# Performance work log

Hardware: AMD Instinct MI355X
Metric: run time of the kernel (lower is better)

Reference implementation:

```python
import jax, jax.numpy as jnp
import numpy as np

B, C, L, O = 32, 256, 336, 96
K, NLAYERS, DFF = 4, 2, 1024
EPS = 1e-5


def setup_inputs() -> dict:
    key = jax.random.key(0)
    ks = jax.random.split(key, 10)
    s1 = 1.0 / np.sqrt(L)
    s2 = 1.0 / np.sqrt(DFF)
    return {
        "x": jax.random.normal(ks[0], (B, C, L), dtype=jnp.float32),
        "rev_w": jnp.ones((C,), dtype=jnp.float32),
        "rev_b": jnp.zeros((C,), dtype=jnp.float32),
        "W1": jax.random.normal(ks[1], (K, NLAYERS, L, DFF), dtype=jnp.float32) * s1,
        "b1": jnp.zeros((K, NLAYERS, DFF), dtype=jnp.float32),
        "W2": jax.random.normal(ks[2], (K, NLAYERS, DFF, L), dtype=jnp.float32) * s2,
        "b2": jnp.zeros((K, NLAYERS, L), dtype=jnp.float32),
        "Wh": jax.random.normal(ks[3], (K, L, O), dtype=jnp.float32) * s1,
        "bh": jnp.zeros((K, O), dtype=jnp.float32),
        "assign": jax.random.randint(ks[4], (C,), 0, K, dtype=jnp.int32),
    }


def reference(x, rev_w, rev_b, W1, b1, W2, b2, Wh, bh, assign):
    # RevIN norm over the time axis, per instance and per channel. x: [B,C,L]
    mean = jnp.mean(x, axis=-1, keepdims=True)
    std = jnp.sqrt(jnp.var(x, axis=-1, keepdims=True) + EPS)
    xn = (x - mean) / std * rev_w[None, :, None] + rev_b[None, :, None]

    n_clusters = Wh.shape[0]
    n_layers = W1.shape[1]
    out = jnp.zeros(x.shape[:2] + (Wh.shape[-1],), dtype=x.dtype)  # [B,C,O]
    for k in range(n_clusters):
        z = xn  # [B,C,L] time-mixing MLP stack shared across channels
        for l in range(n_layers):
            h = jax.nn.relu(jnp.einsum('bcl,ld->bcd', z, W1[k, l]) + b1[k, l])
            z = z + jnp.einsum('bcd,dl->bcl', h, W2[k, l]) + b2[k, l]
        y = jnp.einsum('bcl,lo->bco', z, Wh[k]) + bh[k]  # [B,C,O]
        out = jnp.where((assign == k)[None, :, None], y, out)

    # RevIN denorm, then transpose to [B, out_len, C]
    out = (out - rev_b[None, :, None]) / rev_w[None, :, None] * std + mean
    return jnp.transpose(out, (0, 2, 1))
```

## Files before the change

kernel.cpp:

```cpp
#include <hip/hip_runtime.h>
#include <math.h>


typedef unsigned short u16;
typedef unsigned int u32;
typedef unsigned long long u64;

constexpr int B = 32, C = 256, L = 336, O = 96, K = 4, NL = 2, DFF = 1024;
constexpr int TM = 32;
constexpr int NTILES = (B * C) / TM;
constexpr int LP = 352;
constexpr int ZBS = 360;
constexpr int HS = 1032;

constexpr int DT1 = 32;
constexpr int KT1 = 22;
constexpr int LT2 = 11;
constexpr int KT2 = 64;
constexpr int NTH = 6;
constexpr int KSH = 11;

constexpr int TS1 = KT1 * 512;
constexpr int TS2 = KT2 * 512;
constexpr int THS = KSH * 512;

constexpr int W1FRAGS = DT1 * KT1 * 64;
constexpr int W2FRAGS = LT2 * KT2 * 64;
constexpr int WHFRAGS = NTH * KSH * 64;
constexpr int NW1 = W1FRAGS * K * NL;
constexpr int NW2 = W2FRAGS * K * NL;
constexpr int NPREP = 176 + 256 + 44 + 1;

typedef __bf16 bf16x8 __attribute__((ext_vector_type(8)));
typedef float f32x4 __attribute__((ext_vector_type(4)));
typedef float f32x16 __attribute__((ext_vector_type(16)));

__device__ __forceinline__ u16 f2bf(float f) {
  union { float f; u32 u; } v;
  v.f = f;
  u32 r = v.u + 0x7fffu + ((v.u >> 16) & 1u);
  return (u16)(r >> 16);
}
__device__ __forceinline__ float bf2f(u16 h) {
  union { u32 u; float f; } v;
  v.u = ((u32)h) << 16;
  return v.f;
}
__device__ __forceinline__ u32 pack2(float a, float b) {
  return (u32)f2bf(a) | ((u32)f2bf(b) << 16);
}

__global__ __launch_bounds__(256) void prep(const int* __restrict__ assign,
                                            const float* __restrict__ W1,
                                            const float* __restrict__ W2,
                                            const float* __restrict__ Wh,
                                            int* __restrict__ meta,
                                            u16* __restrict__ wbuf) {
  __shared__ u16 sm[32][516];
  const int bid = blockIdx.x;
  const int tid = threadIdx.x;
  const int wid = tid >> 6, lane = tid & 63;
  const int q = lane >> 4, rm = lane & 15;
  const int q2 = lane >> 5, n32 = lane & 31;

  if (bid < 176) {
    const int dh = bid & 1;
    const int ks32 = (bid >> 1) % 11;
    const int kl = bid / 22;
    for (int rr = 0; rr < 8; ++rr) {
      const int r = wid * 8 + rr;
      const int l = ks32 * 32 + r;
#pragma unroll
      for (int h = 0; h < 2; ++h) {
        const int c = h * 256 + lane * 4;
        float4 v = make_float4(0.f, 0.f, 0.f, 0.f);
        if (l < L)
          v = *(const float4*)(W1 + ((size_t)kl * L + l) * DFF + dh * 512 + c);
        uint2 p;
        p.x = pack2(v.x, v.y);
        p.y = pack2(v.z, v.w);
        *(uint2*)&sm[r][c] = p;
      }
    }
    __syncthreads();
    for (int e = 0; e < 8; ++e) {
      const int item = wid * 8 + e;
      const int dtl = item >> 1, half = item & 1;
      const int rb = 16 * half + q2 * 8;
      const int col = dtl * 32 + n32;
      uint4 o;
      u32 w4[4];
#pragma unroll
      for (int jj = 0; jj < 4; ++jj)
        w4[jj] = (u32)sm[rb + 2 * jj][col] | ((u32)sm[rb + 2 * jj + 1][col] << 16);
      o.x = w4[0]; o.y = w4[1]; o.z = w4[2]; o.w = w4[3];
      const int dt = dh * 16 + dtl;
      const int ks = ks32 * 2 + half;
      *(uint4*)(wbuf + ((size_t)(kl * DT1 + dt) * KT1 + ks) * 512 + lane * 8) = o;
    }
  } else if (bid < 432) {
    const int b2i = bid - 176;
    const int ks32 = b2i & 31;
    const int kl = b2i >> 5;
    for (int rr = 0; rr < 8; ++rr) {
      const int r = wid * 8 + rr;
      const float* row = W2 + ((size_t)kl * DFF + ks32 * 32 + r) * L;
      {
        const int c = lane * 4;
        const float4 v = *(const float4*)(row + c);
        uint2 p;
        p.x = pack2(v.x, v.y);
        p.y = pack2(v.z, v.w);
        *(uint2*)&sm[r][c] = p;
      }
      {
        const int c = 256 + lane * 4;
        if (c < 352) {
          float4 v = make_float4(0.f, 0.f, 0.f, 0.f);
          if (c < L) v = *(const float4*)(row + c);
          uint2 p;
          p.x = pack2(v.x, v.y);
          p.y = pack2(v.z, v.w);
          *(uint2*)&sm[r][c] = p;
        }
      }
    }
    __syncthreads();
    for (int item = wid; item < 22; item += 4) {
      const int lt = item >> 1, half = item & 1;
      const int rb = 16 * half + q2 * 8;
      const int col = 32 * lt + n32;
      uint4 o;
      u32 w4[4];
#pragma unroll
      for (int jj = 0; jj < 4; ++jj)
        w4[jj] = (u32)sm[rb + 2 * jj][col] | ((u32)sm[rb + 2 * jj + 1][col] << 16);
      o.x = w4[0]; o.y = w4[1]; o.z = w4[2]; o.w = w4[3];
      const int ks = ks32 * 2 + half;
      *(uint4*)(wbuf + (size_t)NW1 * 8 +
                ((size_t)(kl * LT2 + lt) * KT2 + ks) * 512 + lane * 8) = o;
    }
  } else if (bid < 476) {
    const int b3i = bid - 432;
    const int ks = b3i % 11;
    const int kk = b3i / 11;
    for (int rr = 0; rr < 8; ++rr) {
      const int r = wid * 8 + rr;
      const int l = ks * 32 + r;
      if (lane < 24) {
        const int c = lane * 4;
        float4 v = make_float4(0.f, 0.f, 0.f, 0.f);
        if (l < L) v = *(const float4*)(Wh + ((size_t)kk * L + l) * O + c);
        uint2 p;
        p.x = pack2(v.x, v.y);
        p.y = pack2(v.z, v.w);
        *(uint2*)&sm[r][c] = p;
      }
    }
    __syncthreads();
    for (int nt = wid; nt < NTH; nt += 4) {
      uint4 o;
      u32 w4[4];
#pragma unroll
      for (int jj = 0; jj < 4; ++jj) {
        const u16 a = sm[q * 8 + 2 * jj][nt * 16 + rm];
        const u16 b = sm[q * 8 + 2 * jj + 1][nt * 16 + rm];
        w4[jj] = (u32)a | ((u32)b << 16);
      }
      o.x = w4[0]; o.y = w4[1]; o.z = w4[2]; o.w = w4[3];
      *(uint4*)(wbuf + (size_t)(NW1 + NW2) * 8 +
                ((size_t)(kk * NTH + nt) * KSH + ks) * 512 + lane * 8) = o;
    }
  } else {
    __shared__ int wcnt[4][K];
    __shared__ int pre[4][K];
    __shared__ int cofs[K + 1];
    const int a = assign[tid];
    const u64 below = (1ull << lane) - 1ull;
    int myrank = 0;
#pragma unroll
    for (int k = 0; k < K; ++k) {
      const u64 m = __ballot(a == k);
      if (a == k) myrank = (int)__popcll(m & below);
      if (lane == 0) wcnt[wid][k] = (int)__popcll(m);
    }
    __syncthreads();
    if (tid == 0) {
      int tot[K];
      for (int k = 0; k < K; ++k) {
        int s = 0;
        for (int ww = 0; ww < 4; ++ww) {
          pre[ww][k] = s;
          s += wcnt[ww][k];
        }
        tot[k] = s;
      }
      cofs[0] = 0;
      for (int k = 0; k < K; ++k) cofs[k + 1] = cofs[k] + tot[k];
      for (int k = 0; k <= K; ++k) meta[512 + k] = cofs[k];
    }
    __syncthreads();
    const int pos = cofs[a] + pre[wid][a] + myrank;
    meta[256 + pos] = tid;
    int k = 0;
    while (k < K - 1 && tid >= cofs[k + 1]) ++k;
    meta[tid] = (k << 16) | ((tid - cofs[k]) * TM);
  }
}

__global__ __launch_bounds__(1024, 4) void mlp_mfma(
    const float* __restrict__ x, const float* __restrict__ rev_w,
    const float* __restrict__ rev_b, const float* __restrict__ b1,
    const float* __restrict__ b2, const float* __restrict__ bh,
    const int* __restrict__ meta, const u16* __restrict__ wbuf,
    float* __restrict__ out) {
  __shared__ __align__(16) u16 zb[TM][ZBS];
  __shared__ __align__(16) u16 Hsh[TM][HS];
  __shared__ float s_mean[TM], s_std[TM], s_rw[TM], s_rb[TM];
  __shared__ int s_b[TM], s_c[TM];

  const int tid = threadIdx.x;
  const int wid = tid >> 6;
  const int lane = tid & 63;
  const int q = lane >> 4, rm = lane & 15;
  const int q2 = lane >> 5, n32 = lane & 31;

  const int swz = (blockIdx.x & 7) * 32 + (blockIdx.x >> 3);
  const int info = meta[swz];
  const int kcl = info >> 16;
  const int rstart = info & 0xffff;
  const int cofs = meta[512 + kcl];
  const int cnt = meta[512 + kcl + 1] - cofs;

  for (int i = 0; i < 2; ++i) {
    const int t = wid * 2 + i;
    const int ri = rstart + t;
    const int b = ri / cnt;
    const int c = meta[256 + cofs + (ri % cnt)];
    const float* xrow = x + (size_t)(b * C + c) * L;
    float v[6], s = 0.f, s2 = 0.f;
#pragma unroll
    for (int jj = 0; jj < 6; ++jj) {
      const int j = lane + jj * 64;
      v[jj] = (j < L) ? xrow[j] : 0.f;
      s += v[jj];
      s2 += v[jj] * v[jj];
    }
#pragma unroll
    for (int off = 32; off > 0; off >>= 1) {
      s += __shfl_down(s, off);
      s2 += __shfl_down(s2, off);
    }
    s = __shfl(s, 0);
    s2 = __shfl(s2, 0);
    const float mean = s * (1.f / L);
    const float var = s2 * (1.f / L) - mean * mean;
    const float stdv = sqrtf(var + 1e-5f);
    const float rstd = 1.f / stdv;
    const float rw = rev_w[c], rb_ = rev_b[c];
#pragma unroll
    for (int jj = 0; jj < 6; ++jj) {
      const int j = lane + jj * 64;
      if (j < L) zb[t][j] = f2bf((v[jj] - mean) * rstd * rw + rb_);
    }
    if (lane < LP - L) zb[t][L + lane] = 0;
    if (lane == 0) {
      s_mean[t] = mean;
      s_std[t] = stdv;
      s_rw[t] = rw;
      s_rb[t] = rb_;
      s_b[t] = b;
      s_c[t] = c;
    }
  }

  const u16* w1b = wbuf;
  const u16* w2b = wbuf + (size_t)NW1 * 8;
  const u16* whb = wbuf + (size_t)(NW1 + NW2) * 8;

  bf16x8 a1[2][4];
  {
    const u16* b0 = w1b + (size_t)(kcl * NL) * W1FRAGS * 8 +
                    (size_t)(wid * 2) * TS1 + lane * 8;
#pragma unroll
    for (int t = 0; t < 2; ++t)
#pragma unroll
      for (int s = 0; s < 4; ++s)
        a1[t][s] = *(const bf16x8*)(b0 + (size_t)t * TS1 + s * 512);
  }
  __syncthreads();

  f32x16 zm;
#pragma unroll
  for (int i = 0; i < 16; ++i) zm[i] = 0.f;
  if (wid < LT2) {
#pragma unroll
    for (int g = 0; g < 4; ++g) {
      const uint2 zw = *(const uint2*)&zb[n32][32 * wid + 8 * g + 4 * q2];
      zm[4 * g + 0] = bf2f((u16)zw.x);
      zm[4 * g + 1] = bf2f((u16)(zw.x >> 16));
      zm[4 * g + 2] = bf2f((u16)zw.y);
      zm[4 * g + 3] = bf2f((u16)(zw.y >> 16));
    }
  }

  for (int l = 0; l < NL; ++l) {
    const int kl = kcl * NL + l;
    const u16* W1f = w1b + (size_t)kl * W1FRAGS * 8;
    const u16* W2f = w2b + (size_t)kl * W2FRAGS * 8;
    const float* b1p = b1 + kl * DFF;
    const float* b2p = b2 + kl * L;
    const u16* base1 = W1f + (size_t)(wid * 2) * TS1 + lane * 8;

    f32x16 acc[2];
#pragma unroll
    for (int t = 0; t < 2; ++t)
#pragma unroll
      for (int i = 0; i < 16; ++i) acc[t][i] = 0.f;
#pragma unroll
    for (int ks = 0; ks < KT1; ++ks) {
      const bf16x8 zf = *(const bf16x8*)&zb[n32][ks * 16 + q2 * 8];
#pragma unroll
      for (int t = 0; t < 2; ++t)
        acc[t] = __builtin_amdgcn_mfma_f32_32x32x16_bf16(a1[t][ks & 3], zf,
                                                         acc[t], 0, 0, 0);
      if (ks + 4 < KT1) {
#pragma unroll
        for (int t = 0; t < 2; ++t)
          a1[t][ks & 3] =
              *(const bf16x8*)(base1 + (size_t)t * TS1 + (ks + 4) * 512);
      }
    }
#pragma unroll
    for (int t = 0; t < 2; ++t) {
      const int dt = wid * 2 + t;
#pragma unroll
      for (int g = 0; g < 4; ++g) {
        const int db = dt * 32 + 8 * g + 4 * q2;
        const float4 bq = *(const float4*)(b1p + db);
        uint2 hw;
        hw.x = pack2(fmaxf(acc[t][4 * g + 0] + bq.x, 0.f),
                     fmaxf(acc[t][4 * g + 1] + bq.y, 0.f));
        hw.y = pack2(fmaxf(acc[t][4 * g + 2] + bq.z, 0.f),
                     fmaxf(acc[t][4 * g + 3] + bq.w, 0.f));
        *(uint2*)&Hsh[n32][db] = hw;
      }
    }

    bf16x8 a2[8];
    const u16* base2 = W2f + (size_t)wid * TS2 + lane * 8;
    if (wid < LT2) {
#pragma unroll
      for (int s = 0; s < 8; ++s)
        a2[s] = *(const bf16x8*)(base2 + s * 512);
    }
    __syncthreads();

    if (wid < LT2) {
#pragma unroll
      for (int ks = 0; ks < KT2; ++ks) {
        const bf16x8 hf = *(const bf16x8*)&Hsh[n32][ks * 16 + q2 * 8];
        zm = __builtin_amdgcn_mfma_f32_32x32x16_bf16(a2[ks & 7], hf, zm, 0, 0, 0);
        if (ks + 8 < KT2)
          a2[ks & 7] = *(const bf16x8*)(base2 + (ks + 8) * 512);
      }
#pragma unroll
      for (int g = 0; g < 4; ++g) {
        const int lc = 32 * wid + 8 * g + 4 * q2;
        if (lc < L) {
          const float4 bq = *(const float4*)(b2p + lc);
          zm[4 * g + 0] += bq.x;
          zm[4 * g + 1] += bq.y;
          zm[4 * g + 2] += bq.z;
          zm[4 * g + 3] += bq.w;
        }
        uint2 zw;
        zw.x = pack2(zm[4 * g + 0], zm[4 * g + 1]);
        zw.y = pack2(zm[4 * g + 2], zm[4 * g + 3]);
        *(uint2*)&zb[n32][lc] = zw;
      }
    }

    if (l + 1 < NL) {
      const u16* nb = w1b + (size_t)(kl + 1) * W1FRAGS * 8 +
                      (size_t)(wid * 2) * TS1 + lane * 8;
#pragma unroll
      for (int t = 0; t < 2; ++t)
#pragma unroll
        for (int s = 0; s < 4; ++s)
          a1[t][s] = *(const bf16x8*)(nb + (size_t)t * TS1 + s * 512);
    }
    __syncthreads();
  }

  if (wid < NTH) {
    const u16* Whf =
        whb + (size_t)kcl * WHFRAGS * 8 + (size_t)wid * THS + lane * 8;
    f32x4 acc0 = {0.f, 0.f, 0.f, 0.f}, acc1 = {0.f, 0.f, 0.f, 0.f};
    for (int ks = 0; ks < KSH; ++ks) {
      const bf16x8 af = *(const bf16x8*)(Whf + ks * 512);
      const bf16x8 zf0 = *(const bf16x8*)&zb[rm][ks * 32 + q * 8];
      const bf16x8 zf1 = *(const bf16x8*)&zb[rm + 16][ks * 32 + q * 8];
      acc0 = __builtin_amdgcn_mfma_f32_16x16x32_bf16(af, zf0, acc0, 0, 0, 0);
      acc1 = __builtin_amdgcn_mfma_f32_16x16x32_bf16(af, zf1, acc1, 0, 0, 0);
    }
    const float4 bq = *(const float4*)(bh + kcl * O + wid * 16 + q * 4);
    const float bqa[4] = {bq.x, bq.y, bq.z, bq.w};
#pragma unroll
    for (int rg = 0; rg < 2; ++rg) {
      const int row = rm + 16 * rg;
      const float mean = s_mean[row], stdv = s_std[row];
      const float rw = s_rw[row], rb_ = s_rb[row];
      const int ob = s_b[row], oc = s_c[row];
      const f32x4 acc = rg ? acc1 : acc0;
#pragma unroll
      for (int gg = 0; gg < 4; ++gg) {
        const int o = wid * 16 + q * 4 + gg;
        const float y = acc[gg] + bqa[gg];
        out[((size_t)ob * O + o) * C + oc] = (y - rb_) / rw * stdv + mean;
      }
    }
  }
}

extern "C" void kernel_launch(void* const* d_in, const int* in_sizes, int n_in,
                              void* d_out, int out_size, void* d_ws,
                              size_t ws_size, hipStream_t stream) {
  const float* x = (const float*)d_in[0];
  const float* rev_w = (const float*)d_in[1];
  const float* rev_b = (const float*)d_in[2];
  const float* W1 = (const float*)d_in[3];
  const float* b1 = (const float*)d_in[4];
  const float* W2 = (const float*)d_in[5];
  const float* b2 = (const float*)d_in[6];
  const float* Wh = (const float*)d_in[7];
  const float* bh = (const float*)d_in[8];
  const int* assign = (const int*)d_in[9];
  float* out = (float*)d_out;

  int* meta = (int*)d_ws;
  u16* wbuf = (u16*)((char*)d_ws + 4096);

  prep<<<NPREP, 256, 0, stream>>>(assign, W1, W2, Wh, meta, wbuf);
  mlp_mfma<<<NTILES, 1024, 0, stream>>>(x, rev_w, rev_b, b1, b2, bh, meta,
                                        wbuf, out);
}
```

Measured before the change: 143.2 us.

## Fuse weight prep and MLP into one cooperative kernel with grid sync

Merges the weight-conversion/prep kernel and the main MFMA MLP kernel into a single cooperatively launched kernel. Each block builds the channel cluster list itself in shared memory, converts two prep units using the Hsh buffer as scratch, computes RevIN stats, then waits at a grid-wide sync before the MLP. This removes a kernel launch boundary and lets weight conversion overlap the x loading. In exchange it adds a grid barrier and relies on all 256 blocks of 1024 threads being co-resident.

New measurement: 202.0 us. 1.41x slower.

```diff
diff --git a/kernel.cpp b/kernel.cpp
--- a/kernel.cpp
+++ b/kernel.cpp
@@ -1,6 +1,9 @@
 #include <hip/hip_runtime.h>
+#include <hip/hip_cooperative_groups.h>
 #include <math.h>
 
+
+namespace cg = cooperative_groups;
 
 typedef unsigned short u16;
 typedef unsigned int u32;
@@ -29,7 +32,9 @@
 constexpr int WHFRAGS = NTH * KSH * 64;
 constexpr int NW1 = W1FRAGS * K * NL;
 constexpr int NW2 = W2FRAGS * K * NL;
-constexpr int NPREP = 176 + 256 + 44 + 1;
+constexpr int NUNITS = 176 + 256 + 44;
+
+constexpr int SMS = 516;
 
 typedef __bf16 bf16x8 __attribute__((ext_vector_type(8)));
 typedef float f32x4 __attribute__((ext_vector_type(4)));
@@ -50,25 +55,83 @@
   return (u32)f2bf(a) | ((u32)f2bf(b) << 16);
 }
 
-__global__ __launch_bounds__(256) void prep(const int* __restrict__ assign,
-                                            const float* __restrict__ W1,
-                                            const float* __restrict__ W2,
-                                            const float* __restrict__ Wh,
-                                            int* __restrict__ meta,
-                                            u16* __restrict__ wbuf) {
-  __shared__ u16 sm[32][516];
-  const int bid = blockIdx.x;
+__global__ __launch_bounds__(1024, 4) void fused(
+    const int* __restrict__ assign, const float* __restrict__ x,
+    const float* __restrict__ rev_w, const float* __restrict__ rev_b,
+    const float* __restrict__ W1, const float* __restrict__ b1,
+    const float* __restrict__ W2, const float* __restrict__ b2,
+    const float* __restrict__ Wh, const float* __restrict__ bh,
+    u16* __restrict__ wbuf, float* __restrict__ out) {
+  __shared__ __align__(16) u16 zb[TM][ZBS];
+  __shared__ __align__(16) u16 Hsh[TM][HS];
+  __shared__ float s_mean[TM], s_std[TM], s_rw[TM], s_rb[TM];
+  __shared__ int s_b[TM], s_c[TM];
+  __shared__ int s_chlist[C];
+  __shared__ int s_cofs[K + 1];
+  __shared__ int s_wcnt[4][K], s_pre[4][K];
+  __shared__ int s_info;
+
   const int tid = threadIdx.x;
-  const int wid = tid >> 6, lane = tid & 63;
+  const int wid = tid >> 6;
+  const int lane = tid & 63;
   const int q = lane >> 4, rm = lane & 15;
   const int q2 = lane >> 5, n32 = lane & 31;
-
-  if (bid < 176) {
-    const int dh = bid & 1;
-    const int ks32 = (bid >> 1) % 11;
-    const int kl = bid / 22;
-    for (int rr = 0; rr < 8; ++rr) {
-      const int r = wid * 8 + rr;
+  const int bid = blockIdx.x;
+
+  const int swz = (bid & 7) * 32 + (bid >> 3);
+
+  const int a = (tid < C) ? assign[tid] : 0;
+  const u64 below = (1ull << lane) - 1ull;
+  int myrank = 0;
+#pragma unroll
+  for (int k = 0; k < K; ++k) {
+    const u64 m = __ballot(tid < C && a == k);
+    if (tid < C && a == k) myrank = (int)__popcll(m & below);
+    if (wid < 4 && lane == 0) s_wcnt[wid][k] = (int)__popcll(m);
+  }
+  __syncthreads();
+  if (tid == 0) {
+    int cofs[K + 1];
+    cofs[0] = 0;
+    for (int k = 0; k < K; ++k) {
+      int s = 0;
+      for (int ww = 0; ww < 4; ++ww) {
+        s_pre[ww][k] = s;
+        s += s_wcnt[ww][k];
+      }
+      cofs[k + 1] = cofs[k] + s;
+    }
+    for (int k = 0; k <= K; ++k) s_cofs[k] = cofs[k];
+    int kk = 0;
+    while (kk < K - 1 && swz >= cofs[kk + 1]) ++kk;
+    s_info = (kk << 16) | ((swz - cofs[kk]) * TM);
+  }
+  __syncthreads();
+  if (tid < C) s_chlist[s_cofs[a] + s_pre[wid][a] + myrank] = tid;
+  __syncthreads();
+
+  const int kcl = s_info >> 16;
+  const int rstart = s_info & 0xffff;
+  const int cofs = s_cofs[kcl];
+  const int cnt = s_cofs[kcl + 1] - cofs;
+
+  const int uu = wid >> 3;
+  const int subwid = wid & 7;
+  const int u = bid * 2 + uu;
+  u16* smu = &Hsh[0][0] + uu * (32 * SMS);
+
+  int utype = -1;
+  if (u < 176) utype = 0;
+  else if (u < 432) utype = 1;
+  else if (u < NUNITS) utype = 2;
+
+  if (utype == 0) {
+    const int dh = u & 1;
+    const int ks32 = (u >> 1) % 11;
+    const int kl = u / 22;
+#pragma unroll
+    for (int rr = 0; rr < 4; ++rr) {
+      const int r = subwid * 4 + rr;
       const int l = ks32 * 32 + r;
 #pragma unroll
       for (int h = 0; h < 2; ++h) {
@@ -79,31 +142,16 @@
         uint2 p;
         p.x = pack2(v.x, v.y);
         p.y = pack2(v.z, v.w);
-        *(uint2*)&sm[r][c] = p;
-      }
-    }
-    __syncthreads();
-    for (int e = 0; e < 8; ++e) {
-      const int item = wid * 8 + e;
-      const int dtl = item >> 1, half = item & 1;
-      const int rb = 16 * half + q2 * 8;
-      const int col = dtl * 32 + n32;
-      uint4 o;
-      u32 w4[4];
-#pragma unroll
-      for (int jj = 0; jj < 4; ++jj)
-        w4[jj] = (u32)sm[rb + 2 * jj][col] | ((u32)sm[rb + 2 * jj + 1][col] << 16);
-      o.x = w4[0]; o.y = w4[1]; o.z = w4[2]; o.w = w4[3];
-      const int dt = dh * 16 + dtl;
-      const int ks = ks32 * 2 + half;
-      *(uint4*)(wbuf + ((size_t)(kl * DT1 + dt) * KT1 + ks) * 512 + lane * 8) = o;
-    }
-  } else if (bid < 432) {
-    const int b2i = bid - 176;
-    const int ks32 = b2i & 31;
-    const int kl = b2i >> 5;
-    for (int rr = 0; rr < 8; ++rr) {
-      const int r = wid * 8 + rr;
+        *(uint2*)&smu[r * SMS + c] = p;
+      }
+    }
+  } else if (utype == 1) {
+    const int g = u - 176;
+    const int ks32 = g & 31;
+    const int kl = g >> 5;
+#pragma unroll
+    for (int rr = 0; rr < 4; ++rr) {
+      const int r = subwid * 4 + rr;
       const float* row = W2 + ((size_t)kl * DFF + ks32 * 32 + r) * L;
       {
         const int c = lane * 4;
@@ -111,7 +159,7 @@
         uint2 p;
         p.x = pack2(v.x, v.y);
         p.y = pack2(v.z, v.w);
-        *(uint2*)&sm[r][c] = p;
+        *(uint2*)&smu[r * SMS + c] = p;
       }
       {
         const int c = 256 + lane * 4;
@@ -121,31 +169,17 @@
           uint2 p;
           p.x = pack2(v.x, v.y);
           p.y = pack2(v.z, v.w);
-          *(uint2*)&sm[r][c] = p;
+          *(uint2*)&smu[r * SMS + c] = p;
         }
       }
     }
-    __syncthreads();
-    for (int item = wid; item < 22; item += 4) {
-      const int lt = item >> 1, half = item & 1;
-      const int rb = 16 * half + q2 * 8;
-      const int col = 32 * lt + n32;
-      uint4 o;
-      u32 w4[4];
-#pragma unroll
-      for (int jj = 0; jj < 4; ++jj)
-        w4[jj] = (u32)sm[rb + 2 * jj][col] | ((u32)sm[rb + 2 * jj + 1][col] << 16);
-      o.x = w4[0]; o.y = w4[1]; o.z = w4[2]; o.w = w4[3];
-      const int ks = ks32 * 2 + half;
-      *(uint4*)(wbuf + (size_t)NW1 * 8 +
-                ((size_t)(kl * LT2 + lt) * KT2 + ks) * 512 + lane * 8) = o;
-    }
-  } else if (bid < 476) {
-    const int b3i = bid - 432;
-    const int ks = b3i % 11;
-    const int kk = b3i / 11;
-    for (int rr = 0; rr < 8; ++rr) {
-      const int r = wid * 8 + rr;
+  } else if (utype == 2) {
+    const int g = u - 432;
+    const int ks = g % 11;
+    const int kk = g / 11;
+#pragma unroll
+    for (int rr = 0; rr < 4; ++rr) {
+      const int r = subwid * 4 + rr;
       const int l = ks * 32 + r;
       if (lane < 24) {
         const int c = lane * 4;
@@ -154,89 +188,77 @@
         uint2 p;
         p.x = pack2(v.x, v.y);
         p.y = pack2(v.z, v.w);
-        *(uint2*)&sm[r][c] = p;
-      }
-    }
-    __syncthreads();
-    for (int nt = wid; nt < NTH; nt += 4) {
+        *(uint2*)&smu[r * SMS + c] = p;
+      }
+    }
+  }
+  __syncthreads();
+
+  if (utype == 0) {
+    const int dh = u & 1;
+    const int ks32 = (u >> 1) % 11;
+    const int kl = u / 22;
+#pragma unroll
+    for (int e = 0; e < 4; ++e) {
+      const int item = subwid * 4 + e;
+      const int dtl = item >> 1, half = item & 1;
+      const int rb = 16 * half + q2 * 8;
+      const int col = dtl * 32 + n32;
       uint4 o;
       u32 w4[4];
 #pragma unroll
+      for (int jj = 0; jj < 4; ++jj)
+        w4[jj] = (u32)smu[(rb + 2 * jj) * SMS + col] |
+                 ((u32)smu[(rb + 2 * jj + 1) * SMS + col] << 16);
+      o.x = w4[0]; o.y = w4[1]; o.z = w4[2]; o.w = w4[3];
+      const int dt = dh * 16 + dtl;
+      const int ks = ks32 * 2 + half;
+      *(uint4*)(wbuf + ((size_t)(kl * DT1 + dt) * KT1 + ks) * 512 + lane * 8) = o;
+    }
+  } else if (utype == 1) {
+    const int g = u - 176;
+    const int ks32 = g & 31;
+    const int kl = g >> 5;
+    for (int item = subwid; item < 22; item += 8) {
+      const int lt = item >> 1, half = item & 1;
+      const int rb = 16 * half + q2 * 8;
+      const int col = 32 * lt + n32;
+      uint4 o;
+      u32 w4[4];
+#pragma unroll
+      for (int jj = 0; jj < 4; ++jj)
+        w4[jj] = (u32)smu[(rb + 2 * jj) * SMS + col] |
+                 ((u32)smu[(rb + 2 * jj + 1) * SMS + col] << 16);
+      o.x = w4[0]; o.y = w4[1]; o.z = w4[2]; o.w = w4[3];
+      const int ks = ks32 * 2 + half;
+      *(uint4*)(wbuf + (size_t)NW1 * 8 +
+                ((size_t)(kl * LT2 + lt) * KT2 + ks) * 512 + lane * 8) = o;
+    }
+  } else if (utype == 2) {
+    const int g = u - 432;
+    const int ks = g % 11;
+    const int kk = g / 11;
+    if (subwid < NTH) {
+      const int nt = subwid;
+      uint4 o;
+      u32 w4[4];
+#pragma unroll
       for (int jj = 0; jj < 4; ++jj) {
-        const u16 a = sm[q * 8 + 2 * jj][nt * 16 + rm];
-        const u16 b = sm[q * 8 + 2 * jj + 1][nt * 16 + rm];
-        w4[jj] = (u32)a | ((u32)b << 16);
+        const u16 aa = smu[(q * 8 + 2 * jj) * SMS + nt * 16 + rm];
+        const u16 bb = smu[(q * 8 + 2 * jj + 1) * SMS + nt * 16 + rm];
+        w4[jj] = (u32)aa | ((u32)bb << 16);
       }
       o.x = w4[0]; o.y = w4[1]; o.z = w4[2]; o.w = w4[3];
       *(uint4*)(wbuf + (size_t)(NW1 + NW2) * 8 +
                 ((size_t)(kk * NTH + nt) * KSH + ks) * 512 + lane * 8) = o;
     }
-  } else {
-    __shared__ int wcnt[4][K];
-    __shared__ int pre[4][K];
-    __shared__ int cofs[K + 1];
-    const int a = assign[tid];
-    const u64 below = (1ull << lane) - 1ull;
-    int myrank = 0;
-#pragma unroll
-    for (int k = 0; k < K; ++k) {
-      const u64 m = __ballot(a == k);
-      if (a == k) myrank = (int)__popcll(m & below);
-      if (lane == 0) wcnt[wid][k] = (int)__popcll(m);
-    }
-    __syncthreads();
-    if (tid == 0) {
-      int tot[K];
-      for (int k = 0; k < K; ++k) {
-        int s = 0;
-        for (int ww = 0; ww < 4; ++ww) {
-          pre[ww][k] = s;
-          s += wcnt[ww][k];
-        }
-        tot[k] = s;
-      }
-      cofs[0] = 0;
-      for (int k = 0; k < K; ++k) cofs[k + 1] = cofs[k] + tot[k];
-      for (int k = 0; k <= K; ++k) meta[512 + k] = cofs[k];
-    }
-    __syncthreads();
-    const int pos = cofs[a] + pre[wid][a] + myrank;
-    meta[256 + pos] = tid;
-    int k = 0;
-    while (k < K - 1 && tid >= cofs[k + 1]) ++k;
-    meta[tid] = (k << 16) | ((tid - cofs[k]) * TM);
-  }
-}
-
-__global__ __launch_bounds__(1024, 4) void mlp_mfma(
-    const float* __restrict__ x, const float* __restrict__ rev_w,
-    const float* __restrict__ rev_b, const float* __restrict__ b1,
-    const float* __restrict__ b2, const float* __restrict__ bh,
-    const int* __restrict__ meta, const u16* __restrict__ wbuf,
-    float* __restrict__ out) {
-  __shared__ __align__(16) u16 zb[TM][ZBS];
-  __shared__ __align__(16) u16 Hsh[TM][HS];
-  __shared__ float s_mean[TM], s_std[TM], s_rw[TM], s_rb[TM];
-  __shared__ int s_b[TM], s_c[TM];
-
-  const int tid = threadIdx.x;
-  const int wid = tid >> 6;
-  const int lane = tid & 63;
-  const int q = lane >> 4, rm = lane & 15;
-  const int q2 = lane >> 5, n32 = lane & 31;
-
-  const int swz = (blockIdx.x & 7) * 32 + (blockIdx.x >> 3);
-  const int info = meta[swz];
-  const int kcl = info >> 16;
-  const int rstart = info & 0xffff;
-  const int cofs = meta[512 + kcl];
-  const int cnt = meta[512 + kcl + 1] - cofs;
+  }
 
   for (int i = 0; i < 2; ++i) {
     const int t = wid * 2 + i;
     const int ri = rstart + t;
     const int b = ri / cnt;
-    const int c = meta[256 + cofs + (ri % cnt)];
+    const int c = s_chlist[cofs + (ri % cnt)];
     const float* xrow = x + (size_t)(b * C + c) * L;
     float v[6], s = 0.f, s2 = 0.f;
 #pragma unroll
@@ -274,6 +296,8 @@
     }
   }
 
+  cg::this_grid().sync();
+
   const u16* w1b = wbuf;
   const u16* w2b = wbuf + (size_t)NW1 * 8;
   const u16* whb = wbuf + (size_t)(NW1 + NW2) * 8;
@@ -288,7 +312,6 @@
       for (int s = 0; s < 4; ++s)
         a1[t][s] = *(const bf16x8*)(b0 + (size_t)t * TS1 + s * 512);
   }
-  __syncthreads();
 
   f32x16 zm;
 #pragma unroll
@@ -351,8 +374,7 @@
     const u16* base2 = W2f + (size_t)wid * TS2 + lane * 8;
     if (wid < LT2) {
 #pragma unroll
-      for (int s = 0; s < 8; ++s)
-        a2[s] = *(const bf16x8*)(base2 + s * 512);
+      for (int s = 0; s < 8; ++s) a2[s] = *(const bf16x8*)(base2 + s * 512);
     }
     __syncthreads();
 
@@ -361,8 +383,7 @@
       for (int ks = 0; ks < KT2; ++ks) {
         const bf16x8 hf = *(const bf16x8*)&Hsh[n32][ks * 16 + q2 * 8];
         zm = __builtin_amdgcn_mfma_f32_32x32x16_bf16(a2[ks & 7], hf, zm, 0, 0, 0);
-        if (ks + 8 < KT2)
-          a2[ks & 7] = *(const bf16x8*)(base2 + (ks + 8) * 512);
+        if (ks + 8 < KT2) a2[ks & 7] = *(const bf16x8*)(base2 + (ks + 8) * 512);
       }
 #pragma unroll
       for (int g = 0; g < 4; ++g) {
@@ -426,6 +447,7 @@
 extern "C" void kernel_launch(void* const* d_in, const int* in_sizes, int n_in,
                               void* d_out, int out_size, void* d_ws,
                               size_t ws_size, hipStream_t stream) {
+  const int* assign = (const int*)d_in[9];
   const float* x = (const float*)d_in[0];
   const float* rev_w = (const float*)d_in[1];
   const float* rev_b = (const float*)d_in[2];
@@ -435,13 +457,12 @@
   const float* b2 = (const float*)d_in[6];
   const float* Wh = (const float*)d_in[7];
   const float* bh = (const float*)d_in[8];
-  const int* assign = (const int*)d_in[9];
   float* out = (float*)d_out;
-
-  int* meta = (int*)d_ws;
-  u16* wbuf = (u16*)((char*)d_ws + 4096);
-
-  prep<<<NPREP, 256, 0, stream>>>(assign, W1, W2, Wh, meta, wbuf);
-  mlp_mfma<<<NTILES, 1024, 0, stream>>>(x, rev_w, rev_b, b1, b2, bh, meta,
-                                        wbuf, out);
+  u16* wbuf = (u16*)d_ws;
+
+  void* args[] = {(void*)&assign, (void*)&x,  (void*)&rev_w, (void*)&rev_b,
+                  (void*)&W1,     (void*)&b1, (void*)&W2,    (void*)&b2,
+                  (void*)&Wh,     (void*)&bh, (void*)&wbuf,  (void*)&out};
+  hipLaunchCooperativeKernel((void*)fused, dim3(NTILES), dim3(1024), args, 0,
+                             stream);
 }
```
